# Kernel optimization log

Measured on AMD Instinct MI355X. Metric: run time of the kernel, lower is better.

Reference implementation:

```python
import jax, jax.numpy as jnp
import numpy as np

EMBED_DIM = 1024
NUM_HEADS = 16
HEAD_DIM = EMBED_DIM // NUM_HEADS
SCALE = HEAD_DIM ** -0.5
B, S = 2, 2048


def setup_inputs() -> dict:
    key = jax.random.key(0)
    ks = jax.random.split(key, 11)
    lim = 1.0 / np.sqrt(EMBED_DIM)
    def lin(kw, kb):
        W = jax.random.uniform(kw, (EMBED_DIM, EMBED_DIM), jnp.float32, -lim, lim)
        b = jax.random.uniform(kb, (EMBED_DIM,), jnp.float32, -lim, lim)
        return W, b
    Wq, bq = lin(ks[0], ks[1])
    Wk, bk = lin(ks[2], ks[3])
    Wv, bv = lin(ks[4], ks[5])
    Wo, bo = lin(ks[6], ks[7])
    query = jax.random.normal(ks[8], (B, S, EMBED_DIM), jnp.float32)
    key_t = jax.random.normal(ks[9], (B, S, EMBED_DIM), jnp.float32)
    value = jax.random.normal(ks[10], (B, S, EMBED_DIM), jnp.float32)
    return {"query": query, "key": key_t, "value": value,
            "Wq": Wq, "bq": bq, "Wk": Wk, "bk": bk,
            "Wv": Wv, "bv": bv, "Wo": Wo, "bo": bo}


def reference(query, key, value, Wq, bq, Wk, bk, Wv, bv, Wo, bo):
    # 'flash' path with attn_mask=None == full softmax attention (chunking is
    # only an execution schedule; per-chunk softmax is over the full key axis).
    b, s, _ = query.shape
    def heads(x, W, bias):
        y = x @ W.T + bias                      # [b, s, E]
        return y.reshape(b, s, NUM_HEADS, HEAD_DIM).transpose(0, 2, 1, 3)  # [b, h, s, d]
    q = heads(query, Wq, bq)
    k = heads(key, Wk, bk)
    v = heads(value, Wv, bv)
    scores = jnp.einsum('bhqd,bhkd->bhqk', q, k) * SCALE
    attn = jax.nn.softmax(scores, axis=-1)
    out = jnp.einsum('bhqk,bhkd->bhqd', attn, v)
    out = out.transpose(0, 2, 1, 3).reshape(b, s, EMBED_DIM)
    return out @ Wo.T + bo
```

## Files before the change

kernel.cpp:

```cpp
#include <hip/hip_runtime.h>

typedef unsigned short u16;
typedef unsigned int u32;
typedef __attribute__((ext_vector_type(8))) __bf16 bf16x8;
typedef __attribute__((ext_vector_type(4))) float f32x4;
typedef __attribute__((ext_vector_type(4))) unsigned short u16x4;
typedef __attribute__((ext_vector_type(8))) unsigned short u16x8;
typedef __attribute__((ext_vector_type(2))) unsigned int u32x2;
typedef __attribute__((ext_vector_type(4))) unsigned int u32x4;

#define DEV static __device__ __forceinline__

DEV void async_copy16(const void* g, void* l) {
  __builtin_amdgcn_global_load_lds((const __attribute__((address_space(1))) void*)g,
                                   (__attribute__((address_space(3))) void*)l, 16, 0, 0);
}
DEV float b2f(u16 s) { union { unsigned u; float f; } v; v.u = ((unsigned)s) << 16; return v.f; }
DEV u16 f2b(float f) {
  union { float f; unsigned u; } v; v.f = f;
  unsigned r = v.u + 0x7FFFu + ((v.u >> 16) & 1u);
  return (u16)(r >> 16);
}
DEV u32 pack2bf(float a, float b) {
  u32 ua = __float_as_uint(a) + 0x8000u;
  u32 ub = __float_as_uint(b) + 0x8000u;
  return __builtin_amdgcn_perm(ub, ua, 0x07060302u);
}

#define MFMA(a, b, c) __builtin_amdgcn_mfma_f32_16x16x32_bf16((a), (b), (c), 0, 0, 0)

__global__ void detect_dtype(const unsigned* __restrict__ q, int* __restrict__ flag) {
  const int lane = threadIdx.x;
  const unsigned w = q[lane];
  const unsigned e = (w >> 7) & 0xFFu;
  const bool inr = (e >= 100u && e <= 132u);
  const unsigned long long m = __ballot(inr);
  if (lane == 0) flag[0] = (__popcll(m) >= 48) ? 1 : 0;
}

__global__ void convert_inputs(
    const void* s0, const void* s1, const void* s2,
    const void* s3, const void* s4, const void* s5, const void* s6,
    const void* s7, const void* s8, const void* s9, const void* s10,
    u16* __restrict__ d0, u16* __restrict__ d1, u16* __restrict__ d2,
    u16* __restrict__ d3, u16* __restrict__ d4, u16* __restrict__ d5, u16* __restrict__ d6,
    float* __restrict__ e7, float* __restrict__ e8, float* __restrict__ e9, float* __restrict__ e10,
    const int* __restrict__ flag)
{
  const int bi = blockIdx.y;
  const void* src = nullptr; u16* db = nullptr; float* df = nullptr; int n = 0;
  switch (bi) {
    case 0:  src = s0;  db = d0; n = 4194304; break;
    case 1:  src = s1;  db = d1; n = 4194304; break;
    case 2:  src = s2;  db = d2; n = 4194304; break;
    case 3:  src = s3;  db = d3; n = 1048576; break;
    case 4:  src = s4;  db = d4; n = 1048576; break;
    case 5:  src = s5;  db = d5; n = 1048576; break;
    case 6:  src = s6;  db = d6; n = 1048576; break;
    case 7:  src = s7;  df = e7; n = 1024; break;
    case 8:  src = s8;  df = e8; n = 1024; break;
    case 9:  src = s9;  df = e9; n = 1024; break;
    default: src = s10; df = e10; n = 1024; break;
  }
  const int isbf = flag[0];
  const int stride = gridDim.x * 256 * 8;
  for (int i = (blockIdx.x * 256 + threadIdx.x) * 8; i < n; i += stride) {
    if (db) {
      u16x8 v;
      if (isbf) {
        v = *(const u16x8*)((const u16*)src + i);
      } else {
        const float* sf = (const float*)src;
#pragma unroll
        for (int j = 0; j < 8; ++j) v[j] = f2b(sf[i + j]);
      }
      *(u16x8*)(db + i) = v;
    } else {
#pragma unroll
      for (int j = 0; j < 8; ++j) {
        float x = isbf ? b2f(((const u16*)src)[i + j]) : ((const float*)src)[i + j];
        df[i + j] = x;
      }
    }
  }
}

__global__ void gemm_qkv(const u16* __restrict__ X0, const u16* __restrict__ X1, const u16* __restrict__ X2,
                         const u16* __restrict__ W0, const u16* __restrict__ W1, const u16* __restrict__ W2,
                         const float* __restrict__ B0, const float* __restrict__ B1, const float* __restrict__ B2,
                         u16* __restrict__ Y0, u16* __restrict__ Y1, u16* __restrict__ Y2,
                         float* __restrict__ Yf, const int* __restrict__ flag, int mode0)
{
  __shared__ __align__(16) u16 smem[17408];

  const int z = blockIdx.z;
  const u16* X  = (z == 0) ? X0 : ((z == 1) ? X1 : X2);
  const u16* W  = (z == 0) ? W0 : ((z == 1) ? W1 : W2);
  const float* Bi = (z == 0) ? B0 : ((z == 1) ? B1 : B2);
  u16* Y        = (z == 0) ? Y0 : ((z == 1) ? Y1 : Y2);
  const int mode = mode0 ? mode0 : z;
  const int outbf = flag[0];

  const int t = threadIdx.x, wave = t >> 6, lane = t & 63;
  const int lane15 = lane & 15, quad = lane >> 4;

  const int L = blockIdx.y * 8 + blockIdx.x;
  const int wrk = (L & 7) * 32 + (L >> 3);
  const int m0 = (wrk >> 3) * 128, n0 = (wrk & 7) * 128;

  const int schunk = (lane & 3) ^ ((lane >> 2) & 3);
  const u16* gA = X + (size_t)(m0 + wave * 16 + (lane >> 2)) * 1024 + schunk * 8;
  const u16* gB = W + (size_t)(n0 + wave * 16 + (lane >> 2)) * 1024 + schunk * 8;

  f32x4 acc[4][4];
#pragma unroll
  for (int i = 0; i < 4; ++i)
#pragma unroll
    for (int j = 0; j < 4; ++j) acc[i][j] = (f32x4){0.f, 0.f, 0.f, 0.f};

  const int wr = wave >> 1, wc = wave & 1;
  const int rchunk = quad ^ (lane15 & 3);

  u16* lA0 = smem + wave * 512;
  u16* lB0 = smem + 4096 + wave * 512;
  u16* lA1 = smem + 8192 + wave * 512;
  u16* lB1 = smem + 12288 + wave * 512;

  auto stage = [&](u16* lA, u16* lB) {
    async_copy16(gA, lA);
    async_copy16(gA + 64 * 1024, lA + 64 * 32);
    async_copy16(gB, lB);
    async_copy16(gB + 64 * 1024, lB + 64 * 32);
    gA += 32; gB += 32;
  };
  auto compute = [&](const u16* As_, const u16* Bs_) {
    bf16x8 af[4], bfv[4];
#pragma unroll
    for (int mt = 0; mt < 4; ++mt)
      af[mt] = *(const bf16x8*)&As_[(wr * 64 + mt * 16 + lane15) * 32 + rchunk * 8];
#pragma unroll
    for (int nt = 0; nt < 4; ++nt)
      bfv[nt] = *(const bf16x8*)&Bs_[(wc * 64 + nt * 16 + lane15) * 32 + rchunk * 8];
    __builtin_amdgcn_s_setprio(1);
#pragma unroll
    for (int mt = 0; mt < 4; ++mt)
#pragma unroll
      for (int nt = 0; nt < 4; ++nt)
        acc[mt][nt] = MFMA(af[mt], bfv[nt], acc[mt][nt]);
    __builtin_amdgcn_s_setprio(0);
  };

  stage(lA0, lB0);
  __syncthreads();

  for (int k0 = 0; k0 < 1024; k0 += 64) {
    if (k0 + 32 < 1024) stage(lA1, lB1);
    compute(smem, smem + 4096);
    __syncthreads();
    if (k0 + 64 < 1024) stage(lA0, lB0);
    compute(smem + 8192, smem + 12288);
    __syncthreads();
  }

  const float qscale = 0.125f * 1.44269504088896340736f;

  if (mode == 2) {
    u16* T2 = smem;
#pragma unroll
    for (int mt = 0; mt < 4; ++mt) {
      const int sl_base = wr * 64 + mt * 16 + quad * 4;
#pragma unroll
      for (int nt = 0; nt < 4; ++nt) {
        const int nn = wc * 64 + nt * 16 + lane15;
        const float bias_v = Bi[n0 + nn];
#pragma unroll
        for (int r = 0; r < 4; ++r) {
          const int sl = sl_base + r;
          const int r5 = sl & 31;
          const int p = (((r5 >> 2) & 3) << 3) | (((r5 >> 4) & 1) << 2) | (r5 & 3);
          T2[nn * 136 + (sl & ~31) + p] = f2b(acc[mt][nt][r] + bias_v);
        }
      }
    }
    __syncthreads();
    const size_t grow0 = (size_t)(m0 >> 11) * 1024 + n0;
    const int col0 = m0 & 2047;
#pragma unroll
    for (int i = 0; i < 8; ++i) {
      const int id = i * 256 + t;
      const int row = id >> 4, ch = id & 15;
      *(u16x8*)&Y[(grow0 + row) * 2048 + col0 + ch * 8] = *(const u16x8*)&T2[row * 136 + ch * 8];
    }
    return;
  }

#pragma unroll
  for (int mt = 0; mt < 4; ++mt) {
    const int m_base = m0 + wr * 64 + mt * 16 + quad * 4;
#pragma unroll
    for (int nt = 0; nt < 4; ++nt) {
      const int n = n0 + wc * 64 + nt * 16 + lane15;
      const float bias_v = Bi[n];
#pragma unroll
      for (int r = 0; r < 4; ++r) {
        const int m = m_base + r;
        float v = acc[mt][nt][r] + bias_v;
        if (mode == 0) v *= qscale;
        if (mode == 3) {
          if (outbf) Y[(size_t)m * 1024 + n] = f2b(v);
          else       Yf[(size_t)m * 1024 + n] = v;
        } else {
          size_t addr = (((size_t)(m >> 11) * 16 + (n >> 6)) * 2048 + (size_t)(m & 2047)) * 64 + (n & 63);
          Y[addr] = f2b(v);
        }
      }
    }
  }
}

__global__ __launch_bounds__(256, 4) void flash_attn(const u16* __restrict__ Qs, const u16* __restrict__ Ks,
                                                     const u16* __restrict__ Vt, u16* __restrict__ AO)
{
  __shared__ __align__(16) u16 smem[16384];
  u16* Kt = smem;
  u16* Vs = smem + 8192;

  const int t = threadIdx.x, wave = t >> 6, lane = t & 63;
  const int lane15 = lane & 15, quad = lane >> 4;
  const int l7 = lane15 & 7;
  const int h = wave >> 1;
  const int c = wave & 1;

  const int Lb = blockIdx.y * 16 + blockIdx.x;
  const int wrk = (Lb & 7) * 128 + (Lb >> 3);
  const int bh = wrk >> 5;
  const int q0 = (wrk & 31) * 64;

  const u16* Qb = Qs + ((size_t)bh * 2048 + q0) * 64;
  const u16* Kb = Ks + (size_t)bh * 2048 * 64;
  const u16* Vb = Vt + (size_t)bh * 64 * 2048;

  const int krow = lane >> 3;
  const int kchunk = (lane & 7) ^ (krow & 7);
  const int vrow = lane >> 4;
  const int vchunk = (lane & 15) ^ (((wave & 1) << 2) + vrow);

#pragma unroll
  for (int r = 0; r < 2; ++r)
    async_copy16(Qb + (size_t)(r * 32 + wave * 8 + krow) * 64 + kchunk * 8,
                 &Kt[(r * 32 + wave * 8) * 64]);
  __syncthreads();
  bf16x8 aq[2][2];
#pragma unroll
  for (int mt = 0; mt < 2; ++mt)
#pragma unroll
    for (int ks = 0; ks < 2; ++ks)
      aq[mt][ks] = *(const bf16x8*)&Kt[(h * 32 + mt * 16 + lane15) * 64 + ((ks * 4 + quad) ^ l7) * 8];
  __syncthreads();

  f32x4 acc_o[2][4];
  f32x4 acc_l[2];
#pragma unroll
  for (int mt = 0; mt < 2; ++mt) {
    acc_l[mt] = (f32x4){0.f, 0.f, 0.f, 0.f};
#pragma unroll
    for (int i = 0; i < 4; ++i) acc_o[mt][i] = (f32x4){0.f, 0.f, 0.f, 0.f};
  }

  u16x8 ou;
#pragma unroll
  for (int j = 0; j < 8; ++j) ou[j] = 0x3F80;
  const bf16x8 ones = __builtin_bit_cast(bf16x8, ou);

  for (int kt = 0; kt < 16; ++kt) {
#pragma unroll
    for (int r = 0; r < 4; ++r)
      async_copy16(Kb + (size_t)(kt * 128 + r * 32 + wave * 8 + krow) * 64 + kchunk * 8,
                   &Kt[(r * 32 + wave * 8) * 64]);
#pragma unroll
    for (int r = 0; r < 4; ++r)
      async_copy16(Vb + (size_t)(r * 16 + wave * 4 + vrow) * 2048 + kt * 128 + vchunk * 8,
                   &Vs[(r * 16 + wave * 4) * 128]);
    __syncthreads();

#pragma unroll
    for (int g = 0; g < 2; ++g) {
      const int ks2 = c * 2 + g;
      bf16x8 bk[2][2];
#pragma unroll
      for (int no = 0; no < 2; ++no)
#pragma unroll
        for (int ks = 0; ks < 2; ++ks)
          bk[no][ks] = *(const bf16x8*)&Kt[(c * 64 + g * 32 + no * 16 + lane15) * 64 + ((ks * 4 + quad) ^ l7) * 8];

      bf16x8 pa[2];
#pragma unroll
      for (int mt = 0; mt < 2; ++mt) {
        f32x4 s2[2];
        s2[0] = (f32x4){0.f, 0.f, 0.f, 0.f};
        s2[1] = (f32x4){0.f, 0.f, 0.f, 0.f};
        __builtin_amdgcn_s_setprio(1);
#pragma unroll
        for (int no = 0; no < 2; ++no)
#pragma unroll
          for (int ks = 0; ks < 2; ++ks)
            s2[no] = MFMA(bk[no][ks], aq[mt][ks], s2[no]);
        __builtin_amdgcn_s_setprio(0);

        float e0[4], e1[4];
#pragma unroll
        for (int rg = 0; rg < 4; ++rg) {
          e0[rg] = __builtin_amdgcn_exp2f(s2[0][rg]);
          e1[rg] = __builtin_amdgcn_exp2f(s2[1][rg]);
        }
        const u32x4 paw = (u32x4){pack2bf(e0[0], e0[1]), pack2bf(e0[2], e0[3]),
                                  pack2bf(e1[0], e1[1]), pack2bf(e1[2], e1[3])};
        pa[mt] = __builtin_bit_cast(bf16x8, paw);
      }

      bf16x8 bv[4];
#pragma unroll
      for (int dt = 0; dt < 4; ++dt)
        bv[dt] = *(const bf16x8*)&Vs[(dt * 16 + lane15) * 128 + ((ks2 * 4 + quad) ^ l7) * 8];
      __builtin_amdgcn_s_setprio(1);
#pragma unroll
      for (int mt = 0; mt < 2; ++mt) {
#pragma unroll
        for (int dt = 0; dt < 4; ++dt)
          acc_o[mt][dt] = MFMA(pa[mt], bv[dt], acc_o[mt][dt]);
        acc_l[mt] = MFMA(pa[mt], ones, acc_l[mt]);
      }
      __builtin_amdgcn_s_setprio(0);
    }
    __syncthreads();
  }

  float* Of = (float*)smem;
  if (c == 1) {
#pragma unroll
    for (int mt = 0; mt < 2; ++mt)
#pragma unroll
      for (int dt = 0; dt < 4; ++dt)
#pragma unroll
        for (int rg = 0; rg < 4; ++rg)
          Of[h * 2048 + (mt * 16 + quad * 4 + rg) * 64 + dt * 16 + lane15] = acc_o[mt][dt][rg];
  }
  __syncthreads();
  if (c == 0) {
#pragma unroll
    for (int mt = 0; mt < 2; ++mt)
#pragma unroll
      for (int dt = 0; dt < 4; ++dt)
#pragma unroll
        for (int rg = 0; rg < 4; ++rg)
          acc_o[mt][dt][rg] += Of[h * 2048 + (mt * 16 + quad * 4 + rg) * 64 + dt * 16 + lane15];
  }
  __syncthreads();
  float* Lf = (float*)smem;
  if (c == 1 && lane15 == 0) {
#pragma unroll
    for (int mt = 0; mt < 2; ++mt)
#pragma unroll
      for (int rg = 0; rg < 4; ++rg)
        Lf[h * 32 + mt * 16 + quad * 4 + rg] = acc_l[mt][rg];
  }
  __syncthreads();
  float rinv[2][4];
  if (c == 0) {
#pragma unroll
    for (int mt = 0; mt < 2; ++mt)
#pragma unroll
      for (int rg = 0; rg < 4; ++rg)
        rinv[mt][rg] = 1.0f / (acc_l[mt][rg] + Lf[h * 32 + mt * 16 + quad * 4 + rg]);
  }
  __syncthreads();

  u16* T = smem;
  if (c == 0) {
#pragma unroll
    for (int mt = 0; mt < 2; ++mt)
#pragma unroll
      for (int dt = 0; dt < 4; ++dt)
#pragma unroll
        for (int rg = 0; rg < 4; ++rg)
          T[(h * 32 + mt * 16 + quad * 4 + rg) * 72 + dt * 16 + lane15] =
              f2b(acc_o[mt][dt][rg] * rinv[mt][rg]);
  }
  __syncthreads();

  const int b = bh >> 4, hh = bh & 15;
#pragma unroll
  for (int i = 0; i < 2; ++i) {
    const int id = i * 256 + t;
    const int row = id >> 3, ch = id & 7;
    *(u16x8*)&AO[((size_t)b * 2048 + q0 + row) * 1024 + hh * 64 + ch * 8] =
        *(const u16x8*)&T[row * 72 + ch * 8];
  }
}

extern "C" void kernel_launch(void* const* d_in, const int* in_sizes, int n_in,
                              void* d_out, int out_size, void* d_ws, size_t ws_size,
                              hipStream_t stream)
{
  const void* query = d_in[0];
  const void* key_  = d_in[1];
  const void* value = d_in[2];
  const void* Wq = d_in[3]; const void* bq = d_in[4];
  const void* Wk = d_in[5]; const void* bk = d_in[6];
  const void* Wv = d_in[7]; const void* bv = d_in[8];
  const void* Wo = d_in[9]; const void* bo = d_in[10];

  u16* ws = (u16*)d_ws;
  u16* Qs  = ws;
  u16* Ks  = Qs + 4194304;
  u16* Vt  = Ks + 4194304;
  u16* AO  = Vt + 4194304;
  u16* Xq  = AO + 4194304;
  u16* Xk  = Xq + 4194304;
  u16* Xv  = Xk + 4194304;
  u16* Wqc = Xv + 4194304;
  u16* Wkc = Wqc + 1048576;
  u16* Wvc = Wkc + 1048576;
  u16* Woc = Wvc + 1048576;
  float* Bc = (float*)(Woc + 1048576);
  int* flag = (int*)(Bc + 4096);

  detect_dtype<<<1, 64, 0, stream>>>((const unsigned*)query, flag);
  convert_inputs<<<dim3(128, 11), 256, 0, stream>>>(
      query, key_, value, Wq, Wk, Wv, Wo, bq, bk, bv, bo,
      Xq, Xk, Xv, Wqc, Wkc, Wvc, Woc,
      Bc, Bc + 1024, Bc + 2048, Bc + 3072, flag);

  gemm_qkv<<<dim3(8, 32, 3), 256, 0, stream>>>(Xq, Xk, Xv, Wqc, Wkc, Wvc,
                                               Bc, Bc + 1024, Bc + 2048,
                                               Qs, Ks, Vt, nullptr, flag, 0);
  flash_attn<<<dim3(16, 64), 256, 0, stream>>>(Qs, Ks, Vt, AO);
  gemm_qkv<<<dim3(8, 32, 1), 256, 0, stream>>>(AO, AO, AO, Woc, Woc, Woc,
                                               Bc + 3072, Bc + 3072, Bc + 3072,
                                               (u16*)d_out, (u16*)d_out, (u16*)d_out,
                                               (float*)d_out, flag, 3);
}
```

Baseline: 222.4 us.

## Fuse fp32-to-bf16 input conversion into GEMM loads and drop conversion kernels

Removes the separate dtype-detect and convert_inputs kernels. The QKV and output GEMMs now read fp32 activations and weights directly, convert them to bf16 in registers with round-to-nearest-even, and write them to LDS. Dtype detection runs inside each GEMM block through a wave ballot. This saves two launches and a full extra read and write of the inputs. In exchange the fp32 path gives up async global-to-LDS copies for register-staged loads, with a write to LDS after each compute step, and the weights are converted again by every block that uses them.

```diff
diff --git a/kernel.cpp b/kernel.cpp
--- a/kernel.cpp
+++ b/kernel.cpp
@@ -26,91 +26,55 @@
   u32 ub = __float_as_uint(b) + 0x8000u;
   return __builtin_amdgcn_perm(ub, ua, 0x07060302u);
 }
-
-#define MFMA(a, b, c) __builtin_amdgcn_mfma_f32_16x16x32_bf16((a), (b), (c), 0, 0, 0)
-
-__global__ void detect_dtype(const unsigned* __restrict__ q, int* __restrict__ flag) {
-  const int lane = threadIdx.x;
-  const unsigned w = q[lane];
-  const unsigned e = (w >> 7) & 0xFFu;
+DEV u32 pack2bf_rne(float a, float b) {
+  u32 ua = __float_as_uint(a); ua += 0x7FFFu + ((ua >> 16) & 1u);
+  u32 ub = __float_as_uint(b); ub += 0x7FFFu + ((ub >> 16) & 1u);
+  return __builtin_amdgcn_perm(ub, ua, 0x07060302u);
+}
+DEV int probe_isbf(const u32* __restrict__ q, int lane) {
+  const u32 w = q[lane & 63];
+  const u32 e = (w >> 7) & 0xFFu;
   const bool inr = (e >= 100u && e <= 132u);
   const unsigned long long m = __ballot(inr);
-  if (lane == 0) flag[0] = (__popcll(m) >= 48) ? 1 : 0;
-}
-
-__global__ void convert_inputs(
-    const void* s0, const void* s1, const void* s2,
-    const void* s3, const void* s4, const void* s5, const void* s6,
-    const void* s7, const void* s8, const void* s9, const void* s10,
-    u16* __restrict__ d0, u16* __restrict__ d1, u16* __restrict__ d2,
-    u16* __restrict__ d3, u16* __restrict__ d4, u16* __restrict__ d5, u16* __restrict__ d6,
-    float* __restrict__ e7, float* __restrict__ e8, float* __restrict__ e9, float* __restrict__ e10,
-    const int* __restrict__ flag)
-{
-  const int bi = blockIdx.y;
-  const void* src = nullptr; u16* db = nullptr; float* df = nullptr; int n = 0;
-  switch (bi) {
-    case 0:  src = s0;  db = d0; n = 4194304; break;
-    case 1:  src = s1;  db = d1; n = 4194304; break;
-    case 2:  src = s2;  db = d2; n = 4194304; break;
-    case 3:  src = s3;  db = d3; n = 1048576; break;
-    case 4:  src = s4;  db = d4; n = 1048576; break;
-    case 5:  src = s5;  db = d5; n = 1048576; break;
-    case 6:  src = s6;  db = d6; n = 1048576; break;
-    case 7:  src = s7;  df = e7; n = 1024; break;
-    case 8:  src = s8;  df = e8; n = 1024; break;
-    case 9:  src = s9;  df = e9; n = 1024; break;
-    default: src = s10; df = e10; n = 1024; break;
-  }
-  const int isbf = flag[0];
-  const int stride = gridDim.x * 256 * 8;
-  for (int i = (blockIdx.x * 256 + threadIdx.x) * 8; i < n; i += stride) {
-    if (db) {
-      u16x8 v;
-      if (isbf) {
-        v = *(const u16x8*)((const u16*)src + i);
-      } else {
-        const float* sf = (const float*)src;
-#pragma unroll
-        for (int j = 0; j < 8; ++j) v[j] = f2b(sf[i + j]);
-      }
-      *(u16x8*)(db + i) = v;
-    } else {
-#pragma unroll
-      for (int j = 0; j < 8; ++j) {
-        float x = isbf ? b2f(((const u16*)src)[i + j]) : ((const float*)src)[i + j];
-        df[i + j] = x;
-      }
-    }
-  }
-}
-
-__global__ void gemm_qkv(const u16* __restrict__ X0, const u16* __restrict__ X1, const u16* __restrict__ X2,
-                         const u16* __restrict__ W0, const u16* __restrict__ W1, const u16* __restrict__ W2,
-                         const float* __restrict__ B0, const float* __restrict__ B1, const float* __restrict__ B2,
+  return (__popcll(m) >= 48) ? 1 : 0;
+}
+
+#define MFMA(a, b, c) __builtin_amdgcn_mfma_f32_16x16x32_bf16((a), (b), (c), 0, 0, 0)
+
+__global__ void gemm_qkv(const void* __restrict__ X0, const void* __restrict__ X1, const void* __restrict__ X2,
+                         const void* __restrict__ W0, const void* __restrict__ W1, const void* __restrict__ W2,
+                         const void* __restrict__ B0, const void* __restrict__ B1, const void* __restrict__ B2,
                          u16* __restrict__ Y0, u16* __restrict__ Y1, u16* __restrict__ Y2,
-                         float* __restrict__ Yf, const int* __restrict__ flag, int mode0)
+                         float* __restrict__ Yf, const u32* __restrict__ det, int mode0)
 {
   __shared__ __align__(16) u16 smem[17408];
 
   const int z = blockIdx.z;
-  const u16* X  = (z == 0) ? X0 : ((z == 1) ? X1 : X2);
-  const u16* W  = (z == 0) ? W0 : ((z == 1) ? W1 : W2);
-  const float* Bi = (z == 0) ? B0 : ((z == 1) ? B1 : B2);
-  u16* Y        = (z == 0) ? Y0 : ((z == 1) ? Y1 : Y2);
+  const void* Xv = (z == 0) ? X0 : ((z == 1) ? X1 : X2);
+  const void* Wv = (z == 0) ? W0 : ((z == 1) ? W1 : W2);
+  const void* Bv = (z == 0) ? B0 : ((z == 1) ? B1 : B2);
+  u16* Y         = (z == 0) ? Y0 : ((z == 1) ? Y1 : Y2);
   const int mode = mode0 ? mode0 : z;
-  const int outbf = flag[0];
 
   const int t = threadIdx.x, wave = t >> 6, lane = t & 63;
   const int lane15 = lane & 15, quad = lane >> 4;
+
+  const int isbf = probe_isbf(det, lane);
+  const int isf32 = !isbf;
+  const int aF = (mode0 == 3) ? 0 : isf32;
+  const int bF = isf32;
 
   const int L = blockIdx.y * 8 + blockIdx.x;
   const int wrk = (L & 7) * 32 + (L >> 3);
   const int m0 = (wrk >> 3) * 128, n0 = (wrk & 7) * 128;
 
   const int schunk = (lane & 3) ^ ((lane >> 2) & 3);
-  const u16* gA = X + (size_t)(m0 + wave * 16 + (lane >> 2)) * 1024 + schunk * 8;
-  const u16* gB = W + (size_t)(n0 + wave * 16 + (lane >> 2)) * 1024 + schunk * 8;
+  const size_t arow = (size_t)(m0 + wave * 16 + (lane >> 2)) * 1024 + schunk * 8;
+  const size_t brow = (size_t)(n0 + wave * 16 + (lane >> 2)) * 1024 + schunk * 8;
+  const u16* uA = (const u16*)Xv + arow;
+  const u16* uB = (const u16*)Wv + brow;
+  const float* fA = (const float*)Xv + arow;
+  const float* fB = (const float*)Wv + brow;
 
   f32x4 acc[4][4];
 #pragma unroll
@@ -126,13 +90,36 @@
   u16* lA1 = smem + 8192 + wave * 512;
   u16* lB1 = smem + 12288 + wave * 512;
 
-  auto stage = [&](u16* lA, u16* lB) {
-    async_copy16(gA, lA);
-    async_copy16(gA + 64 * 1024, lA + 64 * 32);
-    async_copy16(gB, lB);
-    async_copy16(gB + 64 * 1024, lB + 64 * 32);
-    gA += 32; gB += 32;
+  f32x4 pA[4], pB[4];
+  auto loadF32 = [&](int k0) {
+    if (aF) {
+      pA[0] = *(const f32x4*)(fA + k0);         pA[1] = *(const f32x4*)(fA + k0 + 4);
+      pA[2] = *(const f32x4*)(fA + k0 + 65536); pA[3] = *(const f32x4*)(fA + k0 + 65540);
+    }
+    if (bF) {
+      pB[0] = *(const f32x4*)(fB + k0);         pB[1] = *(const f32x4*)(fB + k0 + 4);
+      pB[2] = *(const f32x4*)(fB + k0 + 65536); pB[3] = *(const f32x4*)(fB + k0 + 65540);
+    }
   };
+  auto cvt8 = [&](const f32x4& x, const f32x4& y) -> u32x4 {
+    return (u32x4){pack2bf_rne(x[0], x[1]), pack2bf_rne(x[2], x[3]),
+                   pack2bf_rne(y[0], y[1]), pack2bf_rne(y[2], y[3])};
+  };
+  auto writeF32 = [&](u16* lA, u16* lB) {
+    if (aF) {
+      *(u32x4*)&lA[lane * 8] = cvt8(pA[0], pA[1]);
+      *(u32x4*)&lA[2048 + lane * 8] = cvt8(pA[2], pA[3]);
+    }
+    if (bF) {
+      *(u32x4*)&lB[lane * 8] = cvt8(pB[0], pB[1]);
+      *(u32x4*)&lB[2048 + lane * 8] = cvt8(pB[2], pB[3]);
+    }
+  };
+  auto stageB16 = [&](int k0, u16* lA, u16* lB) {
+    if (!aF) { async_copy16(uA + k0, lA); async_copy16(uA + k0 + 65536, lA + 2048); }
+    if (!bF) { async_copy16(uB + k0, lB); async_copy16(uB + k0 + 65536, lB + 2048); }
+  };
+
   auto compute = [&](const u16* As_, const u16* Bs_) {
     bf16x8 af[4], bfv[4];
 #pragma unroll
@@ -150,19 +137,24 @@
     __builtin_amdgcn_s_setprio(0);
   };
 
-  stage(lA0, lB0);
+  stageB16(0, lA0, lB0);
+  if (aF | bF) { loadF32(0); writeF32(lA0, lB0); }
   __syncthreads();
 
   for (int k0 = 0; k0 < 1024; k0 += 64) {
-    if (k0 + 32 < 1024) stage(lA1, lB1);
+    if (k0 + 32 < 1024) { stageB16(k0 + 32, lA1, lB1); if (aF | bF) loadF32(k0 + 32); }
     compute(smem, smem + 4096);
+    if (k0 + 32 < 1024 && (aF | bF)) writeF32(lA1, lB1);
     __syncthreads();
-    if (k0 + 64 < 1024) stage(lA0, lB0);
+    if (k0 + 64 < 1024) { stageB16(k0 + 64, lA0, lB0); if (aF | bF) loadF32(k0 + 64); }
     compute(smem + 8192, smem + 12288);
+    if (k0 + 64 < 1024 && (aF | bF)) writeF32(lA0, lB0);
     __syncthreads();
   }
 
   const float qscale = 0.125f * 1.44269504088896340736f;
+  const float* BfP = (const float*)Bv;
+  const u16* BuP = (const u16*)Bv;
 
   if (mode == 2) {
     u16* T2 = smem;
@@ -172,7 +164,7 @@
 #pragma unroll
       for (int nt = 0; nt < 4; ++nt) {
         const int nn = wc * 64 + nt * 16 + lane15;
-        const float bias_v = Bi[n0 + nn];
+        const float bias_v = isf32 ? BfP[n0 + nn] : b2f(BuP[n0 + nn]);
 #pragma unroll
         for (int r = 0; r < 4; ++r) {
           const int sl = sl_base + r;
@@ -200,15 +192,15 @@
 #pragma unroll
     for (int nt = 0; nt < 4; ++nt) {
       const int n = n0 + wc * 64 + nt * 16 + lane15;
-      const float bias_v = Bi[n];
+      const float bias_v = isf32 ? BfP[n] : b2f(BuP[n]);
 #pragma unroll
       for (int r = 0; r < 4; ++r) {
         const int m = m_base + r;
         float v = acc[mt][nt][r] + bias_v;
         if (mode == 0) v *= qscale;
         if (mode == 3) {
-          if (outbf) Y[(size_t)m * 1024 + n] = f2b(v);
-          else       Yf[(size_t)m * 1024 + n] = v;
+          if (isbf) Y[(size_t)m * 1024 + n] = f2b(v);
+          else      Yf[(size_t)m * 1024 + n] = v;
         } else {
           size_t addr = (((size_t)(m >> 11) * 16 + (n >> 6)) * 2048 + (size_t)(m & 2047)) * 64 + (n & 63);
           Y[addr] = f2b(v);
@@ -415,28 +407,14 @@
   u16* Ks  = Qs + 4194304;
   u16* Vt  = Ks + 4194304;
   u16* AO  = Vt + 4194304;
-  u16* Xq  = AO + 4194304;
-  u16* Xk  = Xq + 4194304;
-  u16* Xv  = Xk + 4194304;
-  u16* Wqc = Xv + 4194304;
-  u16* Wkc = Wqc + 1048576;
-  u16* Wvc = Wkc + 1048576;
-  u16* Woc = Wvc + 1048576;
-  float* Bc = (float*)(Woc + 1048576);
-  int* flag = (int*)(Bc + 4096);
-
-  detect_dtype<<<1, 64, 0, stream>>>((const unsigned*)query, flag);
-  convert_inputs<<<dim3(128, 11), 256, 0, stream>>>(
-      query, key_, value, Wq, Wk, Wv, Wo, bq, bk, bv, bo,
-      Xq, Xk, Xv, Wqc, Wkc, Wvc, Woc,
-      Bc, Bc + 1024, Bc + 2048, Bc + 3072, flag);
-
-  gemm_qkv<<<dim3(8, 32, 3), 256, 0, stream>>>(Xq, Xk, Xv, Wqc, Wkc, Wvc,
-                                               Bc, Bc + 1024, Bc + 2048,
-                                               Qs, Ks, Vt, nullptr, flag, 0);
+
+  gemm_qkv<<<dim3(8, 32, 3), 256, 0, stream>>>(query, key_, value, Wq, Wk, Wv,
+                                               bq, bk, bv,
+                                               Qs, Ks, Vt, nullptr,
+                                               (const u32*)query, 0);
   flash_attn<<<dim3(16, 64), 256, 0, stream>>>(Qs, Ks, Vt, AO);
-  gemm_qkv<<<dim3(8, 32, 1), 256, 0, stream>>>(AO, AO, AO, Woc, Woc, Woc,
-                                               Bc + 3072, Bc + 3072, Bc + 3072,
+  gemm_qkv<<<dim3(8, 32, 1), 256, 0, stream>>>(AO, AO, AO, Wo, Wo, Wo,
+                                               bo, bo, bo,
                                                (u16*)d_out, (u16*)d_out, (u16*)d_out,
-                                               (float*)d_out, flag, 3);
-}
+                                               (float*)d_out, (const u32*)query, 3);
+}
```

Result: slower. 343.3 us (+54.4%).
